# Optimization experiments

Measured on AMD Instinct MI355X. Metric: run time of the kernel, lower is better.

## Reference

```python
import jax, jax.numpy as jnp
import numpy as np

B, S, D = 64, 2048, 512
N_FINE = 16
MAX_SPANS = 512


def setup_inputs() -> dict:
    key = jax.random.key(0)
    k1, k2, k3 = jax.random.split(key, 3)
    hidden_layers = jax.random.normal(k1, (B, S, D), dtype=jnp.float32)
    slot_embs = jax.random.normal(k2, (D, N_FINE), dtype=jnp.float32)
    # BIO-style coarse tag ids; 1 == B tag, 2 == I tag, others = O / other coarse tags
    bin_labels = jax.random.randint(k3, (B, S), 0, 9, dtype=jnp.int32)
    return {
        "hidden_layers": hidden_layers,
        "slot_embs": slot_embs,
        "bin_labels": bin_labels,
        "coarse_B_index": 1,
        "coarse_I_index": 2,
        "max_spans": MAX_SPANS,
    }


def reference(hidden_layers, slot_embs, bin_labels, coarse_B_index, coarse_I_index, max_spans):
    # Faithful to FinePredictor with enc_type not in {trs, lstm}:
    # span j feature = hidden[B_j] + sum(hidden at I-tagged positions between B_j and B_{j+1});
    # I tokens before the first B tag are dropped (original code skips them).
    # Ragged per-sample span lists are padded to [B, max_spans] (zeros for absent spans).
    bsz, seqlen, d = hidden_layers.shape
    isB = bin_labels == coarse_B_index
    isI = bin_labels == coarse_I_index
    seg = jnp.cumsum(isB.astype(jnp.int32), axis=1) - 1  # span id per token, -1 before first B
    valid = (isB | isI) & (seg >= 0) & (seg < max_spans)
    batch_off = jnp.arange(bsz, dtype=jnp.int32)[:, None] * max_spans
    dummy = bsz * max_spans  # trash segment for invalid tokens
    seg_id = jnp.where(valid, seg + batch_off, dummy)
    feats = jax.ops.segment_sum(
        hidden_layers.reshape(bsz * seqlen, d),
        seg_id.reshape(-1),
        num_segments=dummy + 1,
    )[:-1].reshape(bsz, max_spans, d)
    # score each span feature against the fine slot-name embeddings
    preds = jnp.einsum("bkd,df->bkf", feats, slot_embs)
    return preds
```

## Files before the change

kernel.cpp:

```cpp
#include <hip/hip_runtime.h>
#include <stdint.h>

#define BATCH  64
#define SEQ    2048
#define DIM    512
#define NFINE  16
#define MSPANS 512

__global__ __launch_bounds__(256) void build_spans_kernel(
    const int* __restrict__ labels,
    const int* __restrict__ pB, const int* __restrict__ pI,
    int* __restrict__ count, uint32_t* __restrict__ list,
    float* __restrict__ out)
{
    const int row = blockIdx.x;
    const int tid = threadIdx.x;
    const int Btag = *pB, Itag = *pI;

    float4* oz = (float4*)(out + (size_t)row * MSPANS * NFINE);
    #pragma unroll
    for (int k = 0; k < 8; ++k)
        oz[tid + k * 256] = make_float4(0.f, 0.f, 0.f, 0.f);

    const int4* lab4 = (const int4*)(labels + (size_t)row * SEQ);
    int4 a = lab4[tid * 2], b = lab4[tid * 2 + 1];
    int l[8] = {a.x, a.y, a.z, a.w, b.x, b.y, b.z, b.w};
    int cnt = 0;
    #pragma unroll
    for (int k = 0; k < 8; ++k) cnt += (l[k] == Btag);

    __shared__ int scan[256];
    __shared__ int lcount;
    if (tid == 0) lcount = 0;
    scan[tid] = cnt;
    __syncthreads();
    for (int off = 1; off < 256; off <<= 1) {
        int v = scan[tid];
        int u = (tid >= off) ? scan[tid - off] : 0;
        __syncthreads();
        scan[tid] = v + u;
        __syncthreads();
    }
    int run = (tid > 0) ? scan[tid - 1] : 0;

    uint32_t* lrow = list + (size_t)row * SEQ;
    #pragma unroll
    for (int k = 0; k < 8; ++k) {
        const int  s   = tid * 8 + k;
        const bool isb = (l[k] == Btag);
        const bool isi = (l[k] == Itag);
        run += isb;
        const int seg = run - 1;
        if ((isb | isi) && seg >= 0 && seg < MSPANS) {
            int slot = atomicAdd(&lcount, 1);
            lrow[slot] = ((uint32_t)s << 16) | (uint32_t)seg;
        }
    }
    __syncthreads();
    if (tid == 0) count[row] = lcount;
}

__global__ __launch_bounds__(256) void span_score_kernel(
    const float* __restrict__ hidden,
    const float* __restrict__ semb,
    const int* __restrict__ count,
    const uint32_t* __restrict__ list,
    float* __restrict__ out)
{
    __shared__ float sT[NFINE][DIM + 4];

    for (int i = threadIdx.x; i < DIM * NFINE; i += 256)
        sT[i & 15][i >> 4] = semb[i];
    __syncthreads();

    const int row   = blockIdx.x >> 4;
    const int chunk = blockIdx.x & 15;
    const int wave  = threadIdx.x >> 6;
    const int lane  = threadIdx.x & 63;
    const int t = lane >> 4, f = lane & 15;

    const int n = count[row];
    const float*    hbase = hidden + (size_t)row * SEQ * DIM;
    float*          obase = out    + (size_t)row * MSPANS * NFINE;
    const uint32_t* lrow  = list   + (size_t)row * SEQ;
    const float4*   ev    = (const float4*)&sT[f][0];

    for (int base = (chunk * 4 + wave) * 4; base < n; base += 256) {
        const int idx = base + t;
        if (idx < n) {
            const uint32_t e = lrow[idx];
            const int s   = (int)(e >> 16);
            const int seg = (int)(e & 0xffff);
            const float4* h4 = (const float4*)(hbase + (size_t)s * DIM);
            float a0 = 0.f, a1 = 0.f, a2 = 0.f, a3 = 0.f;
            #pragma unroll 4
            for (int d4 = 0; d4 < DIM / 4; d4 += 2) {
                float4 h0 = h4[d4], h1 = h4[d4 + 1];
                float4 e0 = ev[d4], e1 = ev[d4 + 1];
                a0 = fmaf(h0.x, e0.x, a0);
                a1 = fmaf(h0.y, e0.y, a1);
                a2 = fmaf(h0.z, e0.z, a2);
                a3 = fmaf(h0.w, e0.w, a3);
                a0 = fmaf(h1.x, e1.x, a0);
                a1 = fmaf(h1.y, e1.y, a1);
                a2 = fmaf(h1.z, e1.z, a2);
                a3 = fmaf(h1.w, e1.w, a3);
            }
            const float acc = (a0 + a1) + (a2 + a3);
            atomicAdd(obase + seg * NFINE + f, acc);
        }
    }
}

extern "C" void kernel_launch(void* const* d_in, const int* in_sizes, int n_in,
                              void* d_out, int out_size, void* d_ws, size_t ws_size,
                              hipStream_t stream)
{
    const float* hidden = (const float*)d_in[0];
    const float* semb   = (const float*)d_in[1];
    const int*   labels = (const int*)d_in[2];
    const int*   pB     = (const int*)d_in[3];
    const int*   pI     = (const int*)d_in[4];
    float* out = (float*)d_out;

    int*      count = (int*)d_ws;
    uint32_t* list  = (uint32_t*)((char*)d_ws + 256);

    build_spans_kernel<<<BATCH, 256, 0, stream>>>(labels, pB, pI, count, list, out);
    span_score_kernel<<<BATCH * 16, 256, 0, stream>>>(hidden, semb, count, list, out);
}
```

Before: 355.3 us.

## Split each token's dot product across a wave with shuffle reduction

Each 64-lane wave now processes one token at a time instead of four. The four 16-lane quarters each cover a quarter of the 512-wide hidden row and are combined with xor shuffles, so only one quarter issues the atomic add. Blocks grow to 512 threads, giving 8 waves per block, and the token stride becomes 128. The goal is more memory-level parallelism and better coalescing of the hidden-row reads. The cost is extra shuffle work and a larger block, which can reduce the number of resident blocks.

```diff
diff --git a/kernel.cpp b/kernel.cpp
--- a/kernel.cpp
+++ b/kernel.cpp
@@ -6,6 +6,7 @@
 #define DIM    512
 #define NFINE  16
 #define MSPANS 512
+#define STRIDE 516
 
 __global__ __launch_bounds__(256) void build_spans_kernel(
     const int* __restrict__ labels,
@@ -60,55 +61,49 @@
     if (tid == 0) count[row] = lcount;
 }
 
-__global__ __launch_bounds__(256) void span_score_kernel(
+__global__ __launch_bounds__(512) void span_score_kernel(
     const float* __restrict__ hidden,
     const float* __restrict__ semb,
     const int* __restrict__ count,
     const uint32_t* __restrict__ list,
     float* __restrict__ out)
 {
-    __shared__ float sT[NFINE][DIM + 4];
+    __shared__ float sT[NFINE * STRIDE];
 
-    for (int i = threadIdx.x; i < DIM * NFINE; i += 256)
-        sT[i & 15][i >> 4] = semb[i];
+    for (int i = threadIdx.x; i < DIM * NFINE; i += 512)
+        sT[(i & 15) * STRIDE + (i >> 4)] = semb[i];
     __syncthreads();
 
-    const int row   = blockIdx.x >> 4;
-    const int chunk = blockIdx.x & 15;
-    const int wave  = threadIdx.x >> 6;
-    const int lane  = threadIdx.x & 63;
-    const int t = lane >> 4, f = lane & 15;
+    const int row  = blockIdx.x >> 4;
+    const int wir  = (blockIdx.x & 15) * 8 + (threadIdx.x >> 6);
+    const int lane = threadIdx.x & 63;
+    const int f = lane & 15, q = lane >> 4;
 
     const int n = count[row];
     const float*    hbase = hidden + (size_t)row * SEQ * DIM;
     float*          obase = out    + (size_t)row * MSPANS * NFINE;
     const uint32_t* lrow  = list   + (size_t)row * SEQ;
-    const float4*   ev    = (const float4*)&sT[f][0];
+    const float4*   sv    = (const float4*)&sT[f * STRIDE + q * 128];
 
-    for (int base = (chunk * 4 + wave) * 4; base < n; base += 256) {
-        const int idx = base + t;
-        if (idx < n) {
-            const uint32_t e = lrow[idx];
-            const int s   = (int)(e >> 16);
-            const int seg = (int)(e & 0xffff);
-            const float4* h4 = (const float4*)(hbase + (size_t)s * DIM);
-            float a0 = 0.f, a1 = 0.f, a2 = 0.f, a3 = 0.f;
-            #pragma unroll 4
-            for (int d4 = 0; d4 < DIM / 4; d4 += 2) {
-                float4 h0 = h4[d4], h1 = h4[d4 + 1];
-                float4 e0 = ev[d4], e1 = ev[d4 + 1];
-                a0 = fmaf(h0.x, e0.x, a0);
-                a1 = fmaf(h0.y, e0.y, a1);
-                a2 = fmaf(h0.z, e0.z, a2);
-                a3 = fmaf(h0.w, e0.w, a3);
-                a0 = fmaf(h1.x, e1.x, a0);
-                a1 = fmaf(h1.y, e1.y, a1);
-                a2 = fmaf(h1.z, e1.z, a2);
-                a3 = fmaf(h1.w, e1.w, a3);
-            }
-            const float acc = (a0 + a1) + (a2 + a3);
-            atomicAdd(obase + seg * NFINE + f, acc);
+    for (int idx = wir; idx < n; idx += 128) {
+        const uint32_t e = lrow[idx];
+        const int s   = (int)(e >> 16);
+        const int seg = (int)(e & 0xffff);
+        const float4* h4 = (const float4*)(hbase + (size_t)s * DIM + q * 128);
+        float a0 = 0.f, a1 = 0.f, a2 = 0.f, a3 = 0.f;
+        #pragma unroll 8
+        for (int i = 0; i < 32; ++i) {
+            float4 h  = h4[i];
+            float4 s4 = sv[i];
+            a0 = fmaf(h.x, s4.x, a0);
+            a1 = fmaf(h.y, s4.y, a1);
+            a2 = fmaf(h.z, s4.z, a2);
+            a3 = fmaf(h.w, s4.w, a3);
         }
+        float acc = (a0 + a1) + (a2 + a3);
+        acc += __shfl_xor(acc, 16);
+        acc += __shfl_xor(acc, 32);
+        if (q == 0) atomicAdd(obase + seg * NFINE + f, acc);
     }
 }
 
@@ -127,5 +122,5 @@
     uint32_t* list  = (uint32_t*)((char*)d_ws + 256);
 
     build_spans_kernel<<<BATCH, 256, 0, stream>>>(labels, pB, pI, count, list, out);
-    span_score_kernel<<<BATCH * 16, 256, 0, stream>>>(hidden, semb, count, list, out);
+    span_score_kernel<<<BATCH * 16, 512, 0, stream>>>(hidden, semb, count, list, out);
 }
```

New measurement: 355.4 us. About the same (+0.0%).
